# Optimization experiments

Hardware: AMD Instinct MI355X
Metric: run time of the kernel (lower is better)

The kernel has to match this reference:

```python
import jax, jax.numpy as jnp
import numpy as np

BS, T, D_IN, D_H, D_OUT = 8, 4096, 1024, 1024, 1024


def setup_inputs() -> dict:
    key = jax.random.key(0)
    kx, ka, kb, kc = jax.random.split(key, 4)
    x = jax.random.normal(kx, (BS, T, D_IN), dtype=jnp.float32)
    # stable_init: uniform in [0.999, 1.001)
    a = jax.random.uniform(ka, (D_H,), minval=0.999, maxval=1.001, dtype=jnp.float32)
    # glorot_normal: std = sqrt(2 / (fan_in + fan_out))
    b = jax.random.normal(kb, (D_IN, D_H), dtype=jnp.float32) * np.sqrt(2.0 / (D_IN + D_H))
    c = jax.random.normal(kc, (D_H, D_OUT), dtype=jnp.float32) * np.sqrt(2.0 / (D_H + D_OUT))
    return {"x": x, "a": a, "b": b, "c": c}


def reference(x, a, b, c):
    # Precompute input projection as one big GEMM: u[b,t,h] = x @ b  (input-independent of recurrence)
    u = jnp.einsum('bti,ih->bth', x, b)
    u = jnp.swapaxes(u, 0, 1)  # [T, BS, H] for scan over time

    def step(h, u_t):
        h = h * a + u_t  # diagonal linear recurrence
        return h, h

    init = jnp.zeros((x.shape[0], a.shape[0]), dtype=x.dtype)
    _, hs = jax.lax.scan(step, init, u)  # hs: [T, BS, H]
    # Output projection as one batched GEMM, then back to [BS, T, D_OUT]
    y = jnp.einsum('tbh,ho->bto', hs, c)
    return y
```

## Files before the change

### kernel.cpp

```cpp
#include <hip/hip_runtime.h>
#include <hip/hip_bf16.h>
#include <stdint.h>

#define BS 8
#define TT 4096
#define DI 1024
#define DH 1024
#define DO 1024
#define M1 (BS*TT)
#define NC 64
#define CL (TT/NC)

typedef __attribute__((ext_vector_type(8))) __bf16 bf16x8;
typedef __attribute__((ext_vector_type(4))) __bf16 bf16x4;
typedef __attribute__((ext_vector_type(4))) float f32x4;

__global__ void conv_bf16_kernel(const float* __restrict__ in, __bf16* __restrict__ out, int n8) {
    int i = blockIdx.x * blockDim.x + threadIdx.x;
    int stride = gridDim.x * blockDim.x;
    for (; i < n8; i += stride) {
        f32x4 v0 = *(const f32x4*)&in[(size_t)i * 8];
        f32x4 v1 = *(const f32x4*)&in[(size_t)i * 8 + 4];
        bf16x8 o;
        o[0] = (__bf16)v0[0]; o[1] = (__bf16)v0[1]; o[2] = (__bf16)v0[2]; o[3] = (__bf16)v0[3];
        o[4] = (__bf16)v1[0]; o[5] = (__bf16)v1[1]; o[6] = (__bf16)v1[2]; o[7] = (__bf16)v1[3];
        *(bf16x8*)&out[(size_t)i * 8] = o;
    }
}

__global__ void transp_conv_kernel(const float* __restrict__ src, __bf16* __restrict__ dst,
                                   int K, int N) {
    __shared__ float tile[32][33];
    const int tx = threadIdx.x & 31;
    const int ty = threadIdx.x >> 5;
    const int k0 = blockIdx.x * 32;
    const int n0 = blockIdx.y * 32;
    #pragma unroll
    for (int i = 0; i < 32; i += 8)
        tile[ty + i][tx] = src[(size_t)(k0 + ty + i) * N + n0 + tx];
    __syncthreads();
    #pragma unroll
    for (int i = 0; i < 32; i += 8)
        dst[(size_t)(n0 + ty + i) * K + k0 + tx] = (__bf16)tile[tx][ty + i];
}

template<int OUTF32>
__global__ __launch_bounds__(512, 2) void gemm256_kernel(
    const __bf16* __restrict__ A, const __bf16* __restrict__ Bt,
    __bf16* __restrict__ Obf, float* __restrict__ Of,
    const float* __restrict__ Ea, float* __restrict__ Ep,
    int M, int N, int K)
{
    __shared__ __bf16 lds[65536];
    const int tid = threadIdx.x;
    const int wv = tid >> 6;
    const int l  = tid & 63;
    const int sr = wv >> 2;
    const int sc = wv & 3;
    const int lr = l & 15;
    const int lk = (l >> 4) * 8;
    const int xsw = (lr & 7) * 8;
    const int ak0 = lk ^ xsw, ak1 = (32 + lk) ^ xsw;
    const int rowBase = blockIdx.x * 256;
    const int colBase = blockIdx.y * 256;
    const int aOff = (sr * 64 + lr) * 64;
    const int bOff = (sc * 32 + lr) * 64;
    const int csw = ((l & 7) ^ (l >> 3)) * 8;
    const __bf16* aSrc0 = A  + (size_t)(rowBase + wv * 16 + (l >> 3)) * K + csw;
    const __bf16* bSrc0 = Bt + (size_t)(colBase + wv * 16 + (l >> 3)) * K + csw;

    f32x4 acc[2][2][4][2];
    #pragma unroll
    for (int a0 = 0; a0 < 2; a0++)
        #pragma unroll
        for (int b0 = 0; b0 < 2; b0++)
            #pragma unroll
            for (int m = 0; m < 4; m++)
                #pragma unroll
                for (int n = 0; n < 2; n++)
                    acc[a0][b0][m][n] = (f32x4){0.f, 0.f, 0.f, 0.f};

    bf16x8 aF0[4][2], aF1[4][2], bF[2][2];

#define GLD(s, d) __builtin_amdgcn_global_load_lds( \
        (const __attribute__((address_space(1))) void*)(s), \
        (__attribute__((address_space(3))) void*)(d), 16, 0, 0)
#define STAGE_A(buf, half, ktE) do { \
        const __bf16* s_ = aSrc0 + (size_t)(half) * 128 * K + (ktE); \
        __bf16* d_ = &lds[((buf) * 2 + (half)) * 8192 + wv * 1024]; \
        GLD(s_, d_); GLD(s_ + (size_t)8 * K, d_ + 512); } while (0)
#define STAGE_B(buf, half, ktE) do { \
        const __bf16* s_ = bSrc0 + (size_t)(half) * 128 * K + (ktE); \
        __bf16* d_ = &lds[32768 + ((buf) * 2 + (half)) * 8192 + wv * 1024]; \
        GLD(s_, d_); GLD(s_ + (size_t)8 * K, d_ + 512); } while (0)
#define LOADA(buf, qr, AF) do { \
        const __bf16* Ab_ = &lds[((buf) * 2 + (qr)) * 8192 + aOff]; \
        _Pragma("unroll") \
        for (int m = 0; m < 4; m++) { \
            AF[m][0] = *(const bf16x8*)&Ab_[m * 1024 + ak0]; \
            AF[m][1] = *(const bf16x8*)&Ab_[m * 1024 + ak1]; } } while (0)
#define LOADB(buf, qc) do { \
        const __bf16* Bb_ = &lds[32768 + ((buf) * 2 + (qc)) * 8192 + bOff]; \
        _Pragma("unroll") \
        for (int n = 0; n < 2; n++) { \
            bF[n][0] = *(const bf16x8*)&Bb_[n * 1024 + ak0]; \
            bF[n][1] = *(const bf16x8*)&Bb_[n * 1024 + ak1]; } } while (0)
#define MMQ(qr, qc, AF) do { \
        __builtin_amdgcn_s_setprio(1); \
        _Pragma("unroll") \
        for (int m = 0; m < 4; m++) \
            _Pragma("unroll") \
            for (int n = 0; n < 2; n++) { \
                acc[qr][qc][m][n] = __builtin_amdgcn_mfma_f32_16x16x32_bf16(AF[m][0], bF[n][0], acc[qr][qc][m][n], 0, 0, 0); \
                acc[qr][qc][m][n] = __builtin_amdgcn_mfma_f32_16x16x32_bf16(AF[m][1], bF[n][1], acc[qr][qc][m][n], 0, 0, 0); } \
        __builtin_amdgcn_s_setprio(0); } while (0)
#define PH_BAR() do { __builtin_amdgcn_sched_barrier(0); __builtin_amdgcn_s_barrier(); \
        asm volatile("s_waitcnt lgkmcnt(0)" ::: "memory"); \
        __builtin_amdgcn_sched_barrier(0); } while (0)
#define PHEND() do { __builtin_amdgcn_sched_barrier(0); __builtin_amdgcn_s_barrier(); } while (0)
#define PHEND_W(cond) do { __builtin_amdgcn_sched_barrier(0); \
        if (cond) { asm volatile("s_waitcnt vmcnt(0)" ::: "memory"); } \
        else      { asm volatile("s_waitcnt vmcnt(4)" ::: "memory"); } \
        __builtin_amdgcn_s_barrier(); } while (0)

    const int NIT = K >> 7;

    STAGE_A(0, 0, 0); STAGE_A(0, 1, 0); STAGE_B(0, 0, 0); STAGE_B(0, 1, 0);
    STAGE_A(1, 0, 64); STAGE_A(1, 1, 64); STAGE_B(1, 0, 64); STAGE_B(1, 1, 64);
    asm volatile("s_waitcnt vmcnt(8)" ::: "memory");
    __builtin_amdgcn_s_barrier();

    for (int it = 0; it < NIT; ++it) {
        const int ktOdd  = (2 * it + 1) * 64;
        const int ktEv2  = (2 * it + 2) * 64;
        const int ktOdd2 = (2 * it + 3) * 64;
        const bool last = (it == NIT - 1);
        LOADA(0, 0, aF0); LOADB(0, 0);
        if (it > 0) STAGE_A(1, 1, ktOdd);
        PH_BAR(); MMQ(0, 0, aF0); PHEND();
        LOADA(0, 1, aF1);
        if (it > 0) STAGE_B(1, 1, ktOdd);
        PH_BAR(); MMQ(1, 0, aF1); PHEND();
        LOADB(0, 1);
        if (!last) STAGE_B(0, 0, ktEv2);
        PH_BAR(); MMQ(1, 1, aF1); PHEND();
        if (!last) STAGE_A(0, 0, ktEv2);
        PH_BAR(); MMQ(0, 1, aF0); PHEND_W(last);
        LOADA(1, 0, aF0); LOADB(1, 0);
        if (!last) STAGE_A(0, 1, ktEv2);
        PH_BAR(); MMQ(0, 0, aF0); PHEND();
        LOADA(1, 1, aF1);
        if (!last) STAGE_B(0, 1, ktEv2);
        PH_BAR(); MMQ(1, 0, aF1); PHEND();
        LOADB(1, 1);
        if (!last) STAGE_B(1, 0, ktOdd2);
        PH_BAR(); MMQ(1, 1, aF1); PHEND();
        if (!last) STAGE_A(1, 0, ktOdd2);
        PH_BAR(); MMQ(0, 1, aF0); PHEND_W(last);
    }

    #pragma unroll
    for (int qr = 0; qr < 2; qr++)
        #pragma unroll
        for (int qc = 0; qc < 2; qc++)
            #pragma unroll
            for (int m = 0; m < 4; m++)
                #pragma unroll
                for (int n = 0; n < 2; n++)
                    #pragma unroll
                    for (int j = 0; j < 4; j++) {
                        int row = rowBase + qr * 128 + sr * 64 + m * 16 + (l >> 4) * 4 + j;
                        int col = colBase + qc * 128 + sc * 32 + n * 16 + lr;
                        size_t idx = (size_t)row * N + col;
                        if constexpr (OUTF32) Of[idx] = acc[qr][qc][m][n][j];
                        else                  Obf[idx] = (__bf16)acc[qr][qc][m][n][j];
                    }

    if constexpr (!OUTF32) {
        const int hi = l >> 4;
        const int bb = rowBase >> 12;
        #pragma unroll
        for (int qr = 0; qr < 2; qr++) {
            const int r0 = rowBase + qr * 128 + sr * 64;
            const int kch = (r0 & (TT - 1)) >> 6;
            #pragma unroll
            for (int qc = 0; qc < 2; qc++)
                #pragma unroll
                for (int n = 0; n < 2; n++) {
                    const int ch = colBase + qc * 128 + sc * 32 + n * 16 + lr;
                    const float av = Ea[ch];
                    const float a2 = av * av, a4 = a2 * a2;
                    const float a12 = a4 * a4 * a4;
                    float w = 1.f;
                    if (hi < 3) w *= a4;
                    if (hi < 2) w *= a4;
                    if (hi < 1) w *= a4;
                    float e = 0.f;
                    #pragma unroll
                    for (int m = 3; m >= 0; --m) {
                        #pragma unroll
                        for (int j = 3; j >= 0; --j) {
                            e += w * acc[qr][qc][m][n][j];
                            w *= av;
                        }
                        w *= a12;
                    }
                    e += __shfl_xor(e, 16);
                    e += __shfl_xor(e, 32);
                    if (hi == 0)
                        Ep[((size_t)(bb * NC + kch)) * DH + ch] = e;
                }
        }
    }
#undef GLD
#undef STAGE_A
#undef STAGE_B
#undef LOADA
#undef LOADB
#undef MMQ
#undef PH_BAR
#undef PHEND
#undef PHEND_W
}

__global__ void scan2_kernel(const float* __restrict__ E, const float* __restrict__ a,
                             float* __restrict__ Cc) {
    int g = blockIdx.x * blockDim.x + threadIdx.x;
    int ch = g & (DH - 1);
    int b = g >> 10;
    float av = a[ch];
    float aL = av;
    #pragma unroll
    for (int i = 0; i < 6; i++) aL *= aL;
    float carry = 0.f;
    for (int k = 0; k < NC; k++) {
        size_t idx = ((size_t)(b * NC + k)) * DH + ch;
        Cc[idx] = carry;
        carry = aL * carry + E[idx];
    }
}

__global__ void scan3_kernel(__bf16* __restrict__ u, const float* __restrict__ a,
                             const float* __restrict__ Cc) {
    int g = blockIdx.x * blockDim.x + threadIdx.x;
    int c4 = g & 255;
    int rest = g >> 8;
    int k = rest & (NC - 1);
    int b = rest >> 6;
    int ch = c4 * 4;
    f32x4 av = { a[ch], a[ch + 1], a[ch + 2], a[ch + 3] };
    f32x4 p = *(const f32x4*)&Cc[((size_t)(b * NC + k)) * DH + ch];
    f32x4 h = {0.f, 0.f, 0.f, 0.f};
    size_t base = ((size_t)(b * TT + k * CL)) * DH + ch;
    for (int t = 0; t < CL; t++) {
        size_t idx = base + (size_t)t * DH;
        bf16x4 v = *(bf16x4*)&u[idx];
        h[0] = h[0] * av[0] + (float)v[0];
        h[1] = h[1] * av[1] + (float)v[1];
        h[2] = h[2] * av[2] + (float)v[2];
        h[3] = h[3] * av[3] + (float)v[3];
        p[0] *= av[0]; p[1] *= av[1]; p[2] *= av[2]; p[3] *= av[3];
        bf16x4 o;
        o[0] = (__bf16)(h[0] + p[0]);
        o[1] = (__bf16)(h[1] + p[1]);
        o[2] = (__bf16)(h[2] + p[2]);
        o[3] = (__bf16)(h[3] + p[3]);
        *(bf16x4*)&u[idx] = o;
    }
}

extern "C" void kernel_launch(void* const* d_in, const int* in_sizes, int n_in,
                              void* d_out, int out_size, void* d_ws, size_t ws_size,
                              hipStream_t stream) {
    const float* x = (const float*)d_in[0];
    const float* a = (const float*)d_in[1];
    const float* b = (const float*)d_in[2];
    const float* c = (const float*)d_in[3];
    float* y = (float*)d_out;

    char* ws = (char*)d_ws;
    size_t off = 0;
    __bf16* u  = (__bf16*)(ws + off); off += (size_t)M1 * DH * 2;
    __bf16* bT = (__bf16*)(ws + off); off += (size_t)DI * DH * 2;
    __bf16* cT = (__bf16*)(ws + off); off += (size_t)DH * DO * 2;
    if (ws_size < off) return;

    __bf16* xbf = (__bf16*)d_out;
    float*  E   = (float*)((char*)d_out + (size_t)M1 * DI * 2);
    float*  Cc  = E + (size_t)BS * NC * DH;

    conv_bf16_kernel<<<2048, 256, 0, stream>>>(x, xbf, (M1 * DI) / 8);
    transp_conv_kernel<<<dim3(DI / 32, DH / 32), 256, 0, stream>>>(b, bT, DI, DH);
    transp_conv_kernel<<<dim3(DH / 32, DO / 32), 256, 0, stream>>>(c, cT, DH, DO);
    gemm256_kernel<0><<<dim3(M1 / 256, DH / 256), 512, 0, stream>>>(xbf, bT, u, nullptr, a, E, M1, DH, DI);
    scan2_kernel<<<(BS * DH) / 256, 256, 0, stream>>>(E, a, Cc);
    scan3_kernel<<<(BS * NC * (DH / 4)) / 256, 256, 0, stream>>>(u, a, Cc);
    gemm256_kernel<1><<<dim3(M1 / 256, DO / 256), 512, 0, stream>>>(u, cT, nullptr, y, nullptr, nullptr, M1, DO, DH);
}
```

Before: 218.8 us.

## Fuse fp32-to-bf16 conversion of x into first GEMM's A-tile staging

Removes the separate conversion kernel that wrote a bf16 copy of x. The first GEMM now loads fp32 x tiles into registers, converts them, and writes swizzled bf16 into LDS, interleaved with the existing phase schedule. This saves one full read and write pass over x, but doubles the bytes the first GEMM reads for A. It also replaces the async global-to-LDS loads with register round-trips and explicit LDS writes, which raises register pressure and adds VALU work in the main loop.

```diff
diff --git a/kernel.cpp b/kernel.cpp
--- a/kernel.cpp
+++ b/kernel.cpp
@@ -15,19 +15,6 @@
 typedef __attribute__((ext_vector_type(4))) __bf16 bf16x4;
 typedef __attribute__((ext_vector_type(4))) float f32x4;
 
-__global__ void conv_bf16_kernel(const float* __restrict__ in, __bf16* __restrict__ out, int n8) {
-    int i = blockIdx.x * blockDim.x + threadIdx.x;
-    int stride = gridDim.x * blockDim.x;
-    for (; i < n8; i += stride) {
-        f32x4 v0 = *(const f32x4*)&in[(size_t)i * 8];
-        f32x4 v1 = *(const f32x4*)&in[(size_t)i * 8 + 4];
-        bf16x8 o;
-        o[0] = (__bf16)v0[0]; o[1] = (__bf16)v0[1]; o[2] = (__bf16)v0[2]; o[3] = (__bf16)v0[3];
-        o[4] = (__bf16)v1[0]; o[5] = (__bf16)v1[1]; o[6] = (__bf16)v1[2]; o[7] = (__bf16)v1[3];
-        *(bf16x8*)&out[(size_t)i * 8] = o;
-    }
-}
-
 __global__ void transp_conv_kernel(const float* __restrict__ src, __bf16* __restrict__ dst,
                                    int K, int N) {
     __shared__ float tile[32][33];
@@ -46,7 +33,8 @@
 
 template<int OUTF32>
 __global__ __launch_bounds__(512, 2) void gemm256_kernel(
-    const __bf16* __restrict__ A, const __bf16* __restrict__ Bt,
+    const float* __restrict__ Axf, const __bf16* __restrict__ Ah,
+    const __bf16* __restrict__ Bt,
     __bf16* __restrict__ Obf, float* __restrict__ Of,
     const float* __restrict__ Ea, float* __restrict__ Ep,
     int M, int N, int K)
@@ -66,7 +54,7 @@
     const int aOff = (sr * 64 + lr) * 64;
     const int bOff = (sc * 32 + lr) * 64;
     const int csw = ((l & 7) ^ (l >> 3)) * 8;
-    const __bf16* aSrc0 = A  + (size_t)(rowBase + wv * 16 + (l >> 3)) * K + csw;
+    const __bf16* aSrc0 = OUTF32 ? Ah + (size_t)(rowBase + wv * 16 + (l >> 3)) * K + csw : nullptr;
     const __bf16* bSrc0 = Bt + (size_t)(colBase + wv * 16 + (l >> 3)) * K + csw;
 
     f32x4 acc[2][2][4][2];
@@ -81,6 +69,7 @@
                     acc[a0][b0][m][n] = (f32x4){0.f, 0.f, 0.f, 0.f};
 
     bf16x8 aF0[4][2], aF1[4][2], bF[2][2];
+    f32x4 rA11[4], rA00[4], rA01[4], rA10[4];
 
 #define GLD(s, d) __builtin_amdgcn_global_load_lds( \
         (const __attribute__((address_space(1))) void*)(s), \
@@ -93,6 +82,23 @@
         const __bf16* s_ = bSrc0 + (size_t)(half) * 128 * K + (ktE); \
         __bf16* d_ = &lds[32768 + ((buf) * 2 + (half)) * 8192 + wv * 1024]; \
         GLD(s_, d_); GLD(s_ + (size_t)8 * K, d_ + 512); } while (0)
+#define ALOAD(REG, half, ktE) do { \
+        const float* s_ = Axf + (size_t)(rowBase + (half) * 128 + wv * 16 + (l >> 4)) * K + (ktE) + (l & 15) * 4; \
+        REG[0] = *(const f32x4*)(s_); \
+        REG[1] = *(const f32x4*)(s_ + (size_t)4 * K); \
+        REG[2] = *(const f32x4*)(s_ + (size_t)8 * K); \
+        REG[3] = *(const f32x4*)(s_ + (size_t)12 * K); } while (0)
+#define AWRITE(REG, buf, half) do { \
+        __bf16* db_ = &lds[((buf) * 2 + (half)) * 8192 + wv * 1024]; \
+        const int scb_ = (l & 15) >> 1; const int lh_ = (l & 1); \
+        _Pragma("unroll") \
+        for (int i_ = 0; i_ < 4; i_++) { \
+            int r_ = i_ * 4 + (l >> 4); int j_ = r_ >> 3; int r7_ = r_ & 7; \
+            int d_ = j_ * 512 + (r7_ * 8 + (scb_ ^ r7_)) * 8 + lh_ * 4; \
+            bf16x4 o_; \
+            o_[0] = (__bf16)REG[i_][0]; o_[1] = (__bf16)REG[i_][1]; \
+            o_[2] = (__bf16)REG[i_][2]; o_[3] = (__bf16)REG[i_][3]; \
+            *(bf16x4*)&db_[d_] = o_; } } while (0)
 #define LOADA(buf, qr, AF) do { \
         const __bf16* Ab_ = &lds[((buf) * 2 + (qr)) * 8192 + aOff]; \
         _Pragma("unroll") \
@@ -114,21 +120,30 @@
                 acc[qr][qc][m][n] = __builtin_amdgcn_mfma_f32_16x16x32_bf16(AF[m][0], bF[n][0], acc[qr][qc][m][n], 0, 0, 0); \
                 acc[qr][qc][m][n] = __builtin_amdgcn_mfma_f32_16x16x32_bf16(AF[m][1], bF[n][1], acc[qr][qc][m][n], 0, 0, 0); } \
         __builtin_amdgcn_s_setprio(0); } while (0)
-#define PH_BAR() do { __builtin_amdgcn_sched_barrier(0); __builtin_amdgcn_s_barrier(); \
-        asm volatile("s_waitcnt lgkmcnt(0)" ::: "memory"); \
-        __builtin_amdgcn_sched_barrier(0); } while (0)
-#define PHEND() do { __builtin_amdgcn_sched_barrier(0); __builtin_amdgcn_s_barrier(); } while (0)
-#define PHEND_W(cond) do { __builtin_amdgcn_sched_barrier(0); \
-        if (cond) { asm volatile("s_waitcnt vmcnt(0)" ::: "memory"); } \
-        else      { asm volatile("s_waitcnt vmcnt(4)" ::: "memory"); } \
-        __builtin_amdgcn_s_barrier(); } while (0)
+#define SB __builtin_amdgcn_sched_barrier(0)
+#define BAR __builtin_amdgcn_s_barrier()
+#define LGKM0 asm volatile("s_waitcnt lgkmcnt(0)" ::: "memory")
+#define PH_BAR() do { SB; BAR; LGKM0; SB; } while (0)
+#define PHEND() do { SB; BAR; } while (0)
+#define VMW(cond) do { if (cond) { asm volatile("s_waitcnt vmcnt(0)" ::: "memory"); } \
+                       else      { asm volatile("s_waitcnt vmcnt(4)" ::: "memory"); } } while (0)
 
     const int NIT = K >> 7;
 
-    STAGE_A(0, 0, 0); STAGE_A(0, 1, 0); STAGE_B(0, 0, 0); STAGE_B(0, 1, 0);
-    STAGE_A(1, 0, 64); STAGE_A(1, 1, 64); STAGE_B(1, 0, 64); STAGE_B(1, 1, 64);
-    asm volatile("s_waitcnt vmcnt(8)" ::: "memory");
-    __builtin_amdgcn_s_barrier();
+    if constexpr (!OUTF32) {
+        ALOAD(rA00, 0, 0); ALOAD(rA01, 1, 0);
+        STAGE_B(0, 0, 0); STAGE_B(0, 1, 0);
+        AWRITE(rA00, 0, 0); AWRITE(rA01, 0, 1);
+        ALOAD(rA10, 0, 64); ALOAD(rA11, 1, 64);
+        STAGE_B(1, 0, 64); STAGE_B(1, 1, 64);
+        AWRITE(rA10, 1, 0); AWRITE(rA11, 1, 1);
+        SB; LGKM0; BAR;
+    } else {
+        STAGE_A(0, 0, 0); STAGE_A(0, 1, 0); STAGE_B(0, 0, 0); STAGE_B(0, 1, 0);
+        STAGE_A(1, 0, 64); STAGE_A(1, 1, 64); STAGE_B(1, 0, 64); STAGE_B(1, 1, 64);
+        asm volatile("s_waitcnt vmcnt(8)" ::: "memory");
+        BAR;
+    }
 
     for (int it = 0; it < NIT; ++it) {
         const int ktOdd  = (2 * it + 1) * 64;
@@ -136,7 +151,8 @@
         const int ktOdd2 = (2 * it + 3) * 64;
         const bool last = (it == NIT - 1);
         LOADA(0, 0, aF0); LOADB(0, 0);
-        if (it > 0) STAGE_A(1, 1, ktOdd);
+        if constexpr (!OUTF32) { if (it > 0) ALOAD(rA11, 1, ktOdd); }
+        else                   { if (it > 0) STAGE_A(1, 1, ktOdd); }
         PH_BAR(); MMQ(0, 0, aF0); PHEND();
         LOADA(0, 1, aF1);
         if (it > 0) STAGE_B(1, 1, ktOdd);
@@ -144,10 +160,19 @@
         LOADB(0, 1);
         if (!last) STAGE_B(0, 0, ktEv2);
         PH_BAR(); MMQ(1, 1, aF1); PHEND();
-        if (!last) STAGE_A(0, 0, ktEv2);
-        PH_BAR(); MMQ(0, 1, aF0); PHEND_W(last);
+        if constexpr (!OUTF32) { if (!last) ALOAD(rA00, 0, ktEv2); }
+        else                   { if (!last) STAGE_A(0, 0, ktEv2); }
+        PH_BAR(); MMQ(0, 1, aF0);
+        SB; VMW(last);
+        if constexpr (!OUTF32) { if (it > 0) AWRITE(rA10, 1, 0); }
+        LGKM0; BAR;
         LOADA(1, 0, aF0); LOADB(1, 0);
-        if (!last) STAGE_A(0, 1, ktEv2);
+        if constexpr (!OUTF32) {
+            if (it > 0) AWRITE(rA11, 1, 1);
+            if (!last) ALOAD(rA01, 1, ktEv2);
+        } else {
+            if (!last) STAGE_A(0, 1, ktEv2);
+        }
         PH_BAR(); MMQ(0, 0, aF0); PHEND();
         LOADA(1, 1, aF1);
         if (!last) STAGE_B(0, 1, ktEv2);
@@ -155,8 +180,12 @@
         LOADB(1, 1);
         if (!last) STAGE_B(1, 0, ktOdd2);
         PH_BAR(); MMQ(1, 1, aF1); PHEND();
-        if (!last) STAGE_A(1, 0, ktOdd2);
-        PH_BAR(); MMQ(0, 1, aF0); PHEND_W(last);
+        if constexpr (!OUTF32) { if (!last) ALOAD(rA10, 0, ktOdd2); }
+        else                   { if (!last) STAGE_A(1, 0, ktOdd2); }
+        PH_BAR(); MMQ(0, 1, aF0);
+        SB; VMW(last);
+        if constexpr (!OUTF32) { if (!last) { AWRITE(rA00, 0, 0); AWRITE(rA01, 0, 1); } }
+        LGKM0; BAR;
     }
 
     #pragma unroll
@@ -215,12 +244,17 @@
 #undef GLD
 #undef STAGE_A
 #undef STAGE_B
+#undef ALOAD
+#undef AWRITE
 #undef LOADA
 #undef LOADB
 #undef MMQ
+#undef SB
+#undef BAR
+#undef LGKM0
 #undef PH_BAR
 #undef PHEND
-#undef PHEND_W
+#undef VMW
 }
 
 __global__ void scan2_kernel(const float* __restrict__ E, const float* __restrict__ a,
@@ -285,15 +319,13 @@
     __bf16* cT = (__bf16*)(ws + off); off += (size_t)DH * DO * 2;
     if (ws_size < off) return;
 
-    __bf16* xbf = (__bf16*)d_out;
-    float*  E   = (float*)((char*)d_out + (size_t)M1 * DI * 2);
-    float*  Cc  = E + (size_t)BS * NC * DH;
-
-    conv_bf16_kernel<<<2048, 256, 0, stream>>>(x, xbf, (M1 * DI) / 8);
+    float* E  = (float*)d_out;
+    float* Cc = E + (size_t)BS * NC * DH;
+
     transp_conv_kernel<<<dim3(DI / 32, DH / 32), 256, 0, stream>>>(b, bT, DI, DH);
     transp_conv_kernel<<<dim3(DH / 32, DO / 32), 256, 0, stream>>>(c, cT, DH, DO);
-    gemm256_kernel<0><<<dim3(M1 / 256, DH / 256), 512, 0, stream>>>(xbf, bT, u, nullptr, a, E, M1, DH, DI);
+    gemm256_kernel<0><<<dim3(M1 / 256, DH / 256), 512, 0, stream>>>(x, nullptr, bT, u, nullptr, a, E, M1, DH, DI);
     scan2_kernel<<<(BS * DH) / 256, 256, 0, stream>>>(E, a, Cc);
     scan3_kernel<<<(BS * NC * (DH / 4)) / 256, 256, 0, stream>>>(u, a, Cc);
-    gemm256_kernel<1><<<dim3(M1 / 256, DO / 256), 512, 0, stream>>>(u, cT, nullptr, y, nullptr, nullptr, M1, DO, DH);
-}
+    gemm256_kernel<1><<<dim3(M1 / 256, DO / 256), 512, 0, stream>>>(nullptr, u, cT, nullptr, y, nullptr, nullptr, M1, DO, DH);
+}
```

Result: slower. 326.9 us (+49.4%).
